# Kernel optimization log

Hardware: AMD Instinct MI355X
Metric: run time of the kernel (lower is better)

The kernel has to match this reference:

```python
import jax, jax.numpy as jnp
import numpy as np

B, N, C, H = 4, 128, 512, 8
D = C // H
SCALE = D ** (-0.5) * 50.0


def setup_inputs() -> dict:
    key = jax.random.key(0)
    kx, kw = jax.random.split(key)
    x = jax.random.normal(kx, (B, N, N, C), dtype=jnp.float32)
    # torch Linear(n_embd, 5*n_embd, bias=False); stored here as [in, out] for x @ w
    w_qkv = jax.random.normal(kw, (C, 5 * C), dtype=jnp.float32) * (C ** -0.5)
    return {"x": x, "w_qkv": w_qkv}


def _heads(t):
    # [b, i, j, h*d] -> [b, h, i, j, d]
    b, i, j, _ = t.shape
    return t.reshape(b, i, j, H, D).transpose(0, 3, 1, 2, 4)


def reference(x, w_qkv):
    # global norm over the entire tensor (torch .std() is unbiased, ddof=1)
    x = (x - x.mean()) / x.std(ddof=1)
    qkv = x @ w_qkv                                   # [b, i, j, 5c]
    q, k1, k2, v1, v2 = map(_heads, jnp.split(qkv, 5, axis=-1))
    # pivotal attention: for query (i,j), pivot over k with row stream k1[i,k]
    # and column stream k2[k,j]
    scores = SCALE * (jnp.einsum('bhijd,bhikd->bhijk', q, k1)
                      + jnp.einsum('bhijd,bhkjd->bhijk', q, k2))
    attn = jax.nn.softmax(scores, axis=-1)            # [b, h, i, j, k]
    out = (jnp.einsum('bhijk,bhikd->bhijd', attn, v1)
           + jnp.einsum('bhijk,bhkjd->bhijd', attn, v2))
    # [b, h, i, j, d] -> [b, i, j, h*d]
    return out.transpose(0, 2, 3, 1, 4).reshape(B, N, N, C)
```

## Files before the change

### kernel.cpp

```cpp
#include <hip/hip_runtime.h>
#include <stdint.h>


typedef __attribute__((ext_vector_type(8))) short s8v;
typedef __attribute__((ext_vector_type(4))) float f4v;

#define MFMA(a, b, c) __builtin_amdgcn_mfma_f32_16x16x32_bf16((a), (b), (c), 0, 0, 0)

__device__ __forceinline__ float bf2f(unsigned short u) {
  union { unsigned int i; float f; } v; v.i = ((unsigned int)u) << 16; return v.f;
}
__device__ __forceinline__ unsigned short f2bf(float f) {
  union { float f; unsigned int i; } v; v.f = f;
  unsigned int i = v.i;
  return (unsigned short)((i + 0x7fffu + ((i >> 16) & 1u)) >> 16);
}

__device__ __forceinline__ void async_copy16(const void* g, void* l) {
  __builtin_amdgcn_global_load_lds(
      (const __attribute__((address_space(1))) unsigned int*)(uintptr_t)g,
      (__attribute__((address_space(3))) unsigned int*)(uintptr_t)l,
      16, 0, 0);
}

__global__ __launch_bounds__(256) void k_probe(const unsigned short* __restrict__ x,
                                               int* __restrict__ flag) {
  uint4 v = ((const uint4*)x)[threadIdx.x];
  unsigned int uu[4] = {v.x, v.y, v.z, v.w};
  int bad = 0;
#pragma unroll
  for (int u = 0; u < 4; ++u) {
    float a = bf2f((unsigned short)(uu[u] & 0xffffu));
    float b = bf2f((unsigned short)(uu[u] >> 16));
    if (!(fabsf(a) <= 1e4f)) bad = 1;
    if (!(fabsf(b) <= 1e4f)) bad = 1;
  }
  if (bad) atomicOr(flag, 1);
}

__global__ __launch_bounds__(256) void k_red(const void* __restrict__ xraw,
                                             const int* __restrict__ flag,
                                             double* __restrict__ dstats) {
  __shared__ float red[8];
  const int fm = flag[0];
  int t = threadIdx.x;
  size_t gid = (size_t)blockIdx.x * 256 + t;
  float s = 0.f, ss = 0.f;
  if (fm) {
    const float4* pf = (const float4*)xraw;
#pragma unroll 4
    for (int it = 0; it < 32; ++it) {
      size_t idx = gid + (size_t)it * 131072;
      float4 u1 = pf[2 * idx], u2 = pf[2 * idx + 1];
      float vals[8] = {u1.x, u1.y, u1.z, u1.w, u2.x, u2.y, u2.z, u2.w};
#pragma unroll
      for (int u = 0; u < 8; ++u) { s += vals[u]; ss += vals[u] * vals[u]; }
    }
  } else {
    const uint4* p = (const uint4*)xraw;
#pragma unroll 4
    for (int it = 0; it < 32; ++it) {
      uint4 v = p[gid + (size_t)it * 131072];
      unsigned int uu[4] = {v.x, v.y, v.z, v.w};
#pragma unroll
      for (int u = 0; u < 4; ++u) {
        float a = bf2f((unsigned short)(uu[u] & 0xffffu));
        float b = bf2f((unsigned short)(uu[u] >> 16));
        s += a + b;
        ss += a * a + b * b;
      }
    }
  }
#pragma unroll
  for (int d = 32; d >= 1; d >>= 1) {
    s += __shfl_down(s, d);
    ss += __shfl_down(ss, d);
  }
  int lane = t & 63, wave = t >> 6;
  if (lane == 0) { red[wave] = s; red[4 + wave] = ss; }
  __syncthreads();
  if (t == 0) {
    atomicAdd(&dstats[0], (double)(red[0] + red[1] + red[2] + red[3]));
    atomicAdd(&dstats[1], (double)(red[4] + red[5] + red[6] + red[7]));
  }
}

__global__ void k_stats(const double* __restrict__ dstats, float* __restrict__ fstats) {
  double M = 33554432.0;
  double mean = dstats[0] / M;
  double var = (dstats[1] - dstats[0] * dstats[0] / M) / (M - 1.0);
  double istd = 1.0 / sqrt(var);
  fstats[0] = (float)istd;
  fstats[1] = (float)(-mean * istd);
}

__global__ __launch_bounds__(256) void k_colsum(const void* __restrict__ wraw,
                                                const int* __restrict__ flag,
                                                float* __restrict__ colsum) {
  const int fm = flag[0];
  int c = blockIdx.x * 256 + threadIdx.x;
  if (c >= 2560) return;
  float s = 0.f;
  if (fm) {
    const float* w = (const float*)wraw;
    for (int r = 0; r < 512; ++r) s += w[(size_t)r * 2560 + c];
  } else {
    const unsigned short* w = (const unsigned short*)wraw;
    for (int r = 0; r < 512; ++r) s += bf2f(w[(size_t)r * 2560 + c]);
  }
  colsum[c] = s;
}

__global__ __launch_bounds__(256) void k_wt(const void* __restrict__ wraw,
                                            const int* __restrict__ flag,
                                            unsigned short* __restrict__ wThi,
                                            unsigned short* __restrict__ wTlo) {
  __shared__ float tile[64][65];
  const int fm = flag[0];
  int n0 = blockIdx.x * 64, r0 = blockIdx.y * 64;
#pragma unroll
  for (int rep = 0; rep < 16; ++rep) {
    int idx = rep * 256 + threadIdx.x;
    int r = idx >> 6, n = idx & 63;
    float v;
    if (fm) v = ((const float*)wraw)[(size_t)(r0 + r) * 2560 + n0 + n];
    else    v = bf2f(((const unsigned short*)wraw)[(size_t)(r0 + r) * 2560 + n0 + n]);
    tile[r][n] = v;
  }
  __syncthreads();
#pragma unroll
  for (int rep = 0; rep < 16; ++rep) {
    int idx = rep * 256 + threadIdx.x;
    int n = idx >> 6, r = idx & 63;
    float v = tile[r][n];
    unsigned short hi = f2bf(v);
    size_t o = (size_t)(n0 + n) * 512 + r0 + r;
    wThi[o] = hi;
    wTlo[o] = f2bf(v - bf2f(hi));
  }
}

__global__ __launch_bounds__(256) void k_convx(const void* __restrict__ xraw,
                                               const int* __restrict__ flag,
                                               unsigned short* __restrict__ xhi,
                                               unsigned short* __restrict__ xlo,
                                               int b) {
  const int fm = flag[0];
  size_t e0 = ((size_t)blockIdx.x * 256 + threadIdx.x) * 8;
  size_t g0 = (size_t)b * 8388608 + e0;
  float vals[8];
  if (fm) {
    const float4* pf = (const float4*)xraw;
    float4 u1 = pf[g0 / 4], u2 = pf[g0 / 4 + 1];
    vals[0] = u1.x; vals[1] = u1.y; vals[2] = u1.z; vals[3] = u1.w;
    vals[4] = u2.x; vals[5] = u2.y; vals[6] = u2.z; vals[7] = u2.w;
  } else {
    uint4 v = ((const uint4*)xraw)[g0 / 8];
    unsigned int uu[4] = {v.x, v.y, v.z, v.w};
#pragma unroll
    for (int u = 0; u < 4; ++u) {
      vals[2 * u] = bf2f((unsigned short)(uu[u] & 0xffffu));
      vals[2 * u + 1] = bf2f((unsigned short)(uu[u] >> 16));
    }
  }
  unsigned short h[8], l[8];
#pragma unroll
  for (int u = 0; u < 8; ++u) {
    h[u] = f2bf(vals[u]);
    l[u] = f2bf(vals[u] - bf2f(h[u]));
  }
  *(uint4*)(xhi + e0) = *(const uint4*)h;
  *(uint4*)(xlo + e0) = *(const uint4*)l;
}

__global__ __launch_bounds__(256) void k_gemm(
    const unsigned short* __restrict__ xhi, const unsigned short* __restrict__ xlo,
    const unsigned short* __restrict__ wThi, const unsigned short* __restrict__ wTlo,
    const float* __restrict__ colsum, const float* __restrict__ fstats,
    const int* __restrict__ flag,
    unsigned short* __restrict__ qhi, unsigned short* __restrict__ qlo,
    unsigned short* __restrict__ k1hi, unsigned short* __restrict__ k1lo,
    unsigned short* __restrict__ k2hi, unsigned short* __restrict__ k2lo,
    unsigned short* __restrict__ v1T, unsigned short* __restrict__ v2T,
    int h0, int hcShift) {
  __shared__ __align__(16) unsigned short Ash[128 * 64];
  __shared__ __align__(16) unsigned short Asl[128 * 64];
  __shared__ __align__(16) unsigned short Bsh[128 * 64];
  __shared__ __align__(16) unsigned short Bsl[128 * 64];
  const int fm = flag[0];
  const int t = threadIdx.x;
  const int m0 = blockIdx.x * 128;
  const int n0 = blockIdx.y * 128;
  const int hcMask = (1 << hcShift) - 1;

  const int lane = t & 63, wave = t >> 6;
  const int wm = (wave & 1) * 64, wn = (wave >> 1) * 64;
  const int l16 = lane & 15, q4 = lane >> 4;
  const int srow = t >> 3;
  const int scol = (((t & 7) ^ ((t >> 3) & 7)) * 8);
  const int rsw = l16 & 7;

  const float af = fstats[0], bfc = fstats[1];
  const unsigned short* xh = xhi + (size_t)m0 * 512;
  const unsigned short* xl = xlo + (size_t)m0 * 512;

  int wcolr[4];
#pragma unroll
  for (int r = 0; r < 4; ++r) {
    int ncol = n0 + r * 32 + srow;
    int g = ncol >> hcShift, rem = ncol & hcMask;
    wcolr[r] = (g << 9) + ((h0 + (rem >> 6)) << 6) + (rem & 63);
  }

  f4v acc[4][4];
#pragma unroll
  for (int a = 0; a < 4; ++a)
#pragma unroll
    for (int c = 0; c < 4; ++c) acc[a][c] = (f4v)0.f;

  for (int k0 = 0; k0 < 512; k0 += 64) {
#pragma unroll
    for (int r = 0; r < 4; ++r) {
      int row = r * 32 + srow;
      async_copy16(xh + (size_t)row * 512 + k0 + scol, (char*)Ash + (r * 256 + t) * 16);
    }
#pragma unroll
    for (int r = 0; r < 4; ++r)
      async_copy16(wThi + (size_t)wcolr[r] * 512 + k0 + scol, (char*)Bsh + (r * 256 + t) * 16);
    if (fm) {
#pragma unroll
      for (int r = 0; r < 4; ++r) {
        int row = r * 32 + srow;
        async_copy16(xl + (size_t)row * 512 + k0 + scol, (char*)Asl + (r * 256 + t) * 16);
      }
#pragma unroll
      for (int r = 0; r < 4; ++r)
        async_copy16(wTlo + (size_t)wcolr[r] * 512 + k0 + scol, (char*)Bsl + (r * 256 + t) * 16);
    }
    __syncthreads();
#pragma unroll
    for (int kc = 0; kc < 2; ++kc) {
      const int swoff = ((kc * 4 + q4) ^ rsw) * 8;
      s8v ah[4], bh[4];
#pragma unroll
      for (int jt = 0; jt < 4; ++jt)
        ah[jt] = *(const s8v*)&Ash[(wm + jt * 16 + l16) * 64 + swoff];
#pragma unroll
      for (int nt = 0; nt < 4; ++nt)
        bh[nt] = *(const s8v*)&Bsh[(wn + nt * 16 + l16) * 64 + swoff];
      if (fm) {
        s8v al[4], bl[4];
#pragma unroll
        for (int jt = 0; jt < 4; ++jt)
          al[jt] = *(const s8v*)&Asl[(wm + jt * 16 + l16) * 64 + swoff];
#pragma unroll
        for (int nt = 0; nt < 4; ++nt)
          bl[nt] = *(const s8v*)&Bsl[(wn + nt * 16 + l16) * 64 + swoff];
#pragma unroll
        for (int jt = 0; jt < 4; ++jt)
#pragma unroll
          for (int nt = 0; nt < 4; ++nt) {
            acc[jt][nt] = MFMA(ah[jt], bh[nt], acc[jt][nt]);
            acc[jt][nt] = MFMA(ah[jt], bl[nt], acc[jt][nt]);
            acc[jt][nt] = MFMA(al[jt], bh[nt], acc[jt][nt]);
          }
      } else {
#pragma unroll
        for (int jt = 0; jt < 4; ++jt)
#pragma unroll
          for (int nt = 0; nt < 4; ++nt) acc[jt][nt] = MFMA(ah[jt], bh[nt], acc[jt][nt]);
      }
    }
    __syncthreads();
  }

#pragma unroll
  for (int jt = 0; jt < 4; ++jt) {
#pragma unroll
    for (int nt = 0; nt < 4; ++nt) {
      int gcol = n0 + wn + nt * 16 + l16;
      int g = gcol >> hcShift, rem = gcol & hcMask;
      int hl = rem >> 6, d = rem & 63;
      int wcol = (g << 9) + ((h0 + hl) << 6) + d;
      float cs = colsum[wcol] * bfc;
#pragma unroll
      for (int r = 0; r < 4; ++r) {
        int grow = m0 + wm + jt * 16 + q4 * 4 + r;
        int i = grow >> 7, j = grow & 127;
        float val = acc[jt][nt][r] * af + cs;
        unsigned short hi = f2bf(val);
        if (g == 0) {
          size_t idx = (((size_t)hl * 128 + i) * 128 + j) * 64 + d;
          qhi[idx] = hi; qlo[idx] = f2bf(val - bf2f(hi));
        } else if (g == 1) {
          size_t idx = (((size_t)hl * 128 + i) * 128 + j) * 64 + d;
          k1hi[idx] = hi; k1lo[idx] = f2bf(val - bf2f(hi));
        } else if (g == 2) {
          size_t idx = (((size_t)hl * 128 + j) * 128 + i) * 64 + d;
          k2hi[idx] = hi; k2lo[idx] = f2bf(val - bf2f(hi));
        } else if (g == 3) {
          size_t idx = (((size_t)hl * 128 + i) * 64 + d) * 128 + j;
          v1T[idx] = hi;
        } else {
          size_t idx = (((size_t)hl * 128 + j) * 64 + d) * 128 + i;
          v2T[idx] = hi;
        }
      }
    }
  }
}

__global__ __launch_bounds__(256) void k_s1(
    const unsigned short* __restrict__ qhi, const unsigned short* __restrict__ qlo,
    const unsigned short* __restrict__ k1hi, const unsigned short* __restrict__ k1lo,
    float* __restrict__ S) {
  const int i = blockIdx.x, hl = blockIdx.y;
  const int t = threadIdx.x, lane = t & 63, wave = t >> 6;
  const int l16 = lane & 15, q4 = lane >> 4;
  const size_t base = ((size_t)hl * 128 + i) * 128 * 64;

  f4v acc[2][8];
#pragma unroll
  for (int a = 0; a < 2; ++a)
#pragma unroll
    for (int c = 0; c < 8; ++c) acc[a][c] = (f4v)0.f;

#pragma unroll
  for (int kc = 0; kc < 2; ++kc) {
    s8v ah[2], al[2];
#pragma unroll
    for (int jt = 0; jt < 2; ++jt) {
      size_t off = base + (size_t)(wave * 32 + jt * 16 + l16) * 64 + kc * 32 + q4 * 8;
      ah[jt] = *(const s8v*)(qhi + off);
      al[jt] = *(const s8v*)(qlo + off);
    }
#pragma unroll
    for (int kt = 0; kt < 8; ++kt) {
      size_t off = base + (size_t)(kt * 16 + l16) * 64 + kc * 32 + q4 * 8;
      s8v bh = *(const s8v*)(k1hi + off);
      s8v bl = *(const s8v*)(k1lo + off);
#pragma unroll
      for (int jt = 0; jt < 2; ++jt) {
        acc[jt][kt] = MFMA(ah[jt], bh, acc[jt][kt]);
        acc[jt][kt] = MFMA(ah[jt], bl, acc[jt][kt]);
        acc[jt][kt] = MFMA(al[jt], bh, acc[jt][kt]);
      }
    }
  }
  float* Sb = S + ((size_t)hl * 128 + i) * 128 * 128;
#pragma unroll
  for (int jt = 0; jt < 2; ++jt)
#pragma unroll
    for (int kt = 0; kt < 8; ++kt)
#pragma unroll
      for (int r = 0; r < 4; ++r) {
        int j = wave * 32 + jt * 16 + q4 * 4 + r;
        Sb[(size_t)j * 128 + kt * 16 + l16] = acc[jt][kt][r];
      }
}

__global__ __launch_bounds__(256) void k_s2(
    const unsigned short* __restrict__ qhi, const unsigned short* __restrict__ qlo,
    const unsigned short* __restrict__ k2hi, const unsigned short* __restrict__ k2lo,
    const float* __restrict__ S, unsigned short* __restrict__ attn) {
  const int j = blockIdx.x, hl = blockIdx.y;
  const int t = threadIdx.x, lane = t & 63, wave = t >> 6;
  const int l16 = lane & 15, q4 = lane >> 4;
  const size_t bbase = ((size_t)hl * 128 + j) * 128 * 64;

  f4v acc[2][8];
#pragma unroll
  for (int a = 0; a < 2; ++a)
#pragma unroll
    for (int c = 0; c < 8; ++c) acc[a][c] = (f4v)0.f;

#pragma unroll
  for (int kc = 0; kc < 2; ++kc) {
    s8v ah[2], al[2];
#pragma unroll
    for (int it = 0; it < 2; ++it) {
      size_t off = (((size_t)hl * 128 + (wave * 32 + it * 16 + l16)) * 128 + j) * 64 +
                   kc * 32 + q4 * 8;
      ah[it] = *(const s8v*)(qhi + off);
      al[it] = *(const s8v*)(qlo + off);
    }
#pragma unroll
    for (int kt = 0; kt < 8; ++kt) {
      size_t off = bbase + (size_t)(kt * 16 + l16) * 64 + kc * 32 + q4 * 8;
      s8v bh = *(const s8v*)(k2hi + off);
      s8v bl = *(const s8v*)(k2lo + off);
#pragma unroll
      for (int it = 0; it < 2; ++it) {
        acc[it][kt] = MFMA(ah[it], bh, acc[it][kt]);
        acc[it][kt] = MFMA(ah[it], bl, acc[it][kt]);
        acc[it][kt] = MFMA(al[it], bh, acc[it][kt]);
      }
    }
  }

#pragma unroll
  for (int it = 0; it < 2; ++it) {
#pragma unroll
    for (int r = 0; r < 4; ++r) {
      int i = wave * 32 + it * 16 + q4 * 4 + r;
      const float* Srow = S + (((size_t)hl * 128 + i) * 128 + j) * 128;
      float tv[8];
      float m = -3.4e38f;
#pragma unroll
      for (int kt = 0; kt < 8; ++kt) {
        tv[kt] = 6.25f * (Srow[kt * 16 + l16] + acc[it][kt][r]);
        m = fmaxf(m, tv[kt]);
      }
#pragma unroll
      for (int d = 1; d <= 8; d <<= 1) m = fmaxf(m, __shfl_xor(m, d));
      float sum = 0.f;
#pragma unroll
      for (int kt = 0; kt < 8; ++kt) {
        tv[kt] = __expf(tv[kt] - m);
        sum += tv[kt];
      }
#pragma unroll
      for (int d = 1; d <= 8; d <<= 1) sum += __shfl_xor(sum, d);
      float rs = 1.f / sum;
      unsigned short* arow = attn + (((size_t)hl * 128 + i) * 128 + j) * 128;
#pragma unroll
      for (int kt = 0; kt < 8; ++kt) arow[kt * 16 + l16] = f2bf(tv[kt] * rs);
    }
  }
}

__global__ __launch_bounds__(256) void k_av1(
    const unsigned short* __restrict__ attn, const unsigned short* __restrict__ v1T,
    unsigned short* __restrict__ out1) {
  const int i = blockIdx.x, hl = blockIdx.y;
  const int t = threadIdx.x, lane = t & 63, wave = t >> 6;
  const int l16 = lane & 15, q4 = lane >> 4;
  const size_t abase = ((size_t)hl * 128 + i) * 128 * 128;
  const size_t vbase = ((size_t)hl * 128 + i) * 64 * 128;

  f4v acc[2][4];
#pragma unroll
  for (int a = 0; a < 2; ++a)
#pragma unroll
    for (int c = 0; c < 4; ++c) acc[a][c] = (f4v)0.f;

#pragma unroll
  for (int kc = 0; kc < 4; ++kc) {
    s8v a[2], bfr[4];
#pragma unroll
    for (int jt = 0; jt < 2; ++jt)
      a[jt] = *(const s8v*)(attn + abase + (size_t)(wave * 32 + jt * 16 + l16) * 128 +
                            kc * 32 + q4 * 8);
#pragma unroll
    for (int dt = 0; dt < 4; ++dt)
      bfr[dt] = *(const s8v*)(v1T + vbase + (size_t)(dt * 16 + l16) * 128 + kc * 32 + q4 * 8);
#pragma unroll
    for (int jt = 0; jt < 2; ++jt)
#pragma unroll
      for (int dt = 0; dt < 4; ++dt) acc[jt][dt] = MFMA(a[jt], bfr[dt], acc[jt][dt]);
  }
  unsigned short* ob = out1 + ((size_t)hl * 128 + i) * 128 * 64;
#pragma unroll
  for (int jt = 0; jt < 2; ++jt)
#pragma unroll
    for (int dt = 0; dt < 4; ++dt)
#pragma unroll
      for (int r = 0; r < 4; ++r) {
        int j = wave * 32 + jt * 16 + q4 * 4 + r;
        ob[(size_t)j * 64 + dt * 16 + l16] = f2bf(acc[jt][dt][r]);
      }
}

__global__ __launch_bounds__(256) void k_av2(
    const unsigned short* __restrict__ attn, const unsigned short* __restrict__ v2T,
    const unsigned short* __restrict__ out1, const int* __restrict__ flag,
    void* __restrict__ out, int b, int h0) {
  const int j = blockIdx.x, hl = blockIdx.y;
  const int t = threadIdx.x, lane = t & 63, wave = t >> 6;
  const int l16 = lane & 15, q4 = lane >> 4;
  const int fm = flag[0];
  const size_t vbase = ((size_t)hl * 128 + j) * 64 * 128;

  f4v acc[2][4];
#pragma unroll
  for (int a = 0; a < 2; ++a)
#pragma unroll
    for (int c = 0; c < 4; ++c) acc[a][c] = (f4v)0.f;

#pragma unroll
  for (int kc = 0; kc < 4; ++kc) {
    s8v a[2], bfr[4];
#pragma unroll
    for (int it = 0; it < 2; ++it)
      a[it] = *(const s8v*)(attn +
                            (((size_t)hl * 128 + (wave * 32 + it * 16 + l16)) * 128 + j) * 128 +
                            kc * 32 + q4 * 8);
#pragma unroll
    for (int dt = 0; dt < 4; ++dt)
      bfr[dt] = *(const s8v*)(v2T + vbase + (size_t)(dt * 16 + l16) * 128 + kc * 32 + q4 * 8);
#pragma unroll
    for (int it = 0; it < 2; ++it)
#pragma unroll
      for (int dt = 0; dt < 4; ++dt) acc[it][dt] = MFMA(a[it], bfr[dt], acc[it][dt]);
  }
#pragma unroll
  for (int it = 0; it < 2; ++it)
#pragma unroll
    for (int dt = 0; dt < 4; ++dt)
#pragma unroll
      for (int r = 0; r < 4; ++r) {
        int i = wave * 32 + it * 16 + q4 * 4 + r;
        int d = dt * 16 + l16;
        float o = acc[it][dt][r] + bf2f(out1[(((size_t)hl * 128 + i) * 128 + j) * 64 + d]);
        size_t oi = ((size_t)b * 16384 + i * 128 + j) * 512 + (h0 + hl) * 64 + d;
        if (fm) ((float*)out)[oi] = o;
        else    ((unsigned short*)out)[oi] = f2bf(o);
      }
}

extern "C" void kernel_launch(void* const* d_in, const int* in_sizes, int n_in,
                              void* d_out, int out_size, void* d_ws, size_t ws_size,
                              hipStream_t stream) {
  (void)in_sizes; (void)n_in; (void)out_size;
  const void* x = d_in[0];
  const void* w = d_in[1];

  const size_t xslice = (size_t)16384 * 512;
  const size_t wTsz = (size_t)2560 * 512;
  const size_t fixed = xslice * 4 + wTsz * 4 + 2560 * 4 + 64;

  int Hc = 2;
  if (30 * ((size_t)8 * 1048576) + fixed <= ws_size) Hc = 8;
  else if (30 * ((size_t)4 * 1048576) + fixed <= ws_size) Hc = 4;
  const int hcShift = (Hc == 8) ? 9 : ((Hc == 4) ? 8 : 7);
  const size_t TE = (size_t)Hc * 1048576;

  char* p = (char*)d_ws;
  unsigned short* qhi = (unsigned short*)p;  p += TE * 2;
  unsigned short* qlo = (unsigned short*)p;  p += TE * 2;
  unsigned short* k1hi = (unsigned short*)p; p += TE * 2;
  unsigned short* k1lo = (unsigned short*)p; p += TE * 2;
  unsigned short* k2hi = (unsigned short*)p; p += TE * 2;
  unsigned short* k2lo = (unsigned short*)p; p += TE * 2;
  unsigned short* v1T = (unsigned short*)p;  p += TE * 2;
  unsigned short* v2T = (unsigned short*)p;  p += TE * 2;
  float* S = (float*)p;                      p += TE * 8;
  unsigned short* attn = (unsigned short*)p; p += TE * 4;
  unsigned short* out1 = (unsigned short*)p; p += TE * 2;
  unsigned short* xhi = (unsigned short*)p;  p += xslice * 2;
  unsigned short* xlo = (unsigned short*)p;  p += xslice * 2;
  unsigned short* wThi = (unsigned short*)p; p += wTsz * 2;
  unsigned short* wTlo = (unsigned short*)p; p += wTsz * 2;
  float* colsum = (float*)p;                 p += 2560 * 4;
  double* dstats = (double*)p;               p += 16;
  int* flag = (int*)p;                       p += 8;
  float* fstats = (float*)p;                 p += 8;

  hipMemsetAsync(dstats, 0, 24, stream);
  k_probe<<<1, 256, 0, stream>>>((const unsigned short*)x, flag);
  k_red<<<512, 256, 0, stream>>>(x, flag, dstats);
  k_stats<<<1, 1, 0, stream>>>(dstats, fstats);
  k_colsum<<<10, 256, 0, stream>>>(w, flag, colsum);
  k_wt<<<dim3(40, 8), 256, 0, stream>>>(w, flag, wThi, wTlo);

  for (int b = 0; b < 4; ++b) {
    k_convx<<<4096, 256, 0, stream>>>(x, flag, xhi, xlo, b);
    for (int h0 = 0; h0 < 8; h0 += Hc) {
      k_gemm<<<dim3(128, (5 * Hc * 64) / 128), 256, 0, stream>>>(
          xhi, xlo, wThi, wTlo, colsum, fstats, flag,
          qhi, qlo, k1hi, k1lo, k2hi, k2lo, v1T, v2T, h0, hcShift);
      k_s1<<<dim3(128, Hc), 256, 0, stream>>>(qhi, qlo, k1hi, k1lo, S);
      k_s2<<<dim3(128, Hc), 256, 0, stream>>>(qhi, qlo, k2hi, k2lo, S, attn);
      k_av1<<<dim3(128, Hc), 256, 0, stream>>>(attn, v1T, out1);
      k_av2<<<dim3(128, Hc), 256, 0, stream>>>(attn, v2T, out1, flag, d_out, b, h0);
    }
  }
}
```

Measured before the change: 1.636 ms.

## Double-buffer QKV GEMM LDS tiles with 32-wide K steps

Restructures the projection GEMM main loop to use two LDS buffers with a K step of 32 instead of 64. The next tile's async global-to-LDS copies are issued before the MFMA work on the current buffer, removing one barrier per iteration and overlapping loads with compute. LDS footprint stays the same, but there are twice as many iterations and the swizzle pattern changes to a 4-chunk XOR scheme.

New measurement: 1.672 ms. 1.02x slower.

```diff
diff --git a/kernel.cpp b/kernel.cpp
--- a/kernel.cpp
+++ b/kernel.cpp
@@ -183,10 +183,10 @@
     unsigned short* __restrict__ k2hi, unsigned short* __restrict__ k2lo,
     unsigned short* __restrict__ v1T, unsigned short* __restrict__ v2T,
     int h0, int hcShift) {
-  __shared__ __align__(16) unsigned short Ash[128 * 64];
-  __shared__ __align__(16) unsigned short Asl[128 * 64];
-  __shared__ __align__(16) unsigned short Bsh[128 * 64];
-  __shared__ __align__(16) unsigned short Bsl[128 * 64];
+  __shared__ __align__(16) unsigned short Ash[2][4096];
+  __shared__ __align__(16) unsigned short Asl[2][4096];
+  __shared__ __align__(16) unsigned short Bsh[2][4096];
+  __shared__ __align__(16) unsigned short Bsl[2][4096];
   const int fm = flag[0];
   const int t = threadIdx.x;
   const int m0 = blockIdx.x * 128;
@@ -196,20 +196,22 @@
   const int lane = t & 63, wave = t >> 6;
   const int wm = (wave & 1) * 64, wn = (wave >> 1) * 64;
   const int l16 = lane & 15, q4 = lane >> 4;
-  const int srow = t >> 3;
-  const int scol = (((t & 7) ^ ((t >> 3) & 7)) * 8);
-  const int rsw = l16 & 7;
+
+  const int srow0 = t >> 2;
+  const int srow1 = 64 + srow0;
+  const int sch = (((t & 3) ^ ((t >> 3) & 3)) << 3);
+  const int swoff = ((q4 ^ ((l16 >> 1) & 3)) << 3);
 
   const float af = fstats[0], bfc = fstats[1];
   const unsigned short* xh = xhi + (size_t)m0 * 512;
   const unsigned short* xl = xlo + (size_t)m0 * 512;
 
-  int wcolr[4];
-#pragma unroll
-  for (int r = 0; r < 4; ++r) {
-    int ncol = n0 + r * 32 + srow;
-    int g = ncol >> hcShift, rem = ncol & hcMask;
-    wcolr[r] = (g << 9) + ((h0 + (rem >> 6)) << 6) + (rem & 63);
+  int wcol0, wcol1;
+  {
+    int n = n0 + srow0, g = n >> hcShift, rem = n & hcMask;
+    wcol0 = (g << 9) + ((h0 + (rem >> 6)) << 6) + (rem & 63);
+    n = n0 + srow1; g = n >> hcShift; rem = n & hcMask;
+    wcol1 = (g << 9) + ((h0 + (rem >> 6)) << 6) + (rem & 63);
   }
 
   f4v acc[4][4];
@@ -218,58 +220,55 @@
 #pragma unroll
     for (int c = 0; c < 4; ++c) acc[a][c] = (f4v)0.f;
 
-  for (int k0 = 0; k0 < 512; k0 += 64) {
-#pragma unroll
-    for (int r = 0; r < 4; ++r) {
-      int row = r * 32 + srow;
-      async_copy16(xh + (size_t)row * 512 + k0 + scol, (char*)Ash + (r * 256 + t) * 16);
-    }
-#pragma unroll
-    for (int r = 0; r < 4; ++r)
-      async_copy16(wThi + (size_t)wcolr[r] * 512 + k0 + scol, (char*)Bsh + (r * 256 + t) * 16);
+  auto STAGE = [&](int bsel, int k0) {
+    async_copy16(xh + (size_t)srow0 * 512 + k0 + sch, (char*)&Ash[bsel][0] + t * 16);
+    async_copy16(xh + (size_t)srow1 * 512 + k0 + sch, (char*)&Ash[bsel][0] + (256 + t) * 16);
+    async_copy16(wThi + (size_t)wcol0 * 512 + k0 + sch, (char*)&Bsh[bsel][0] + t * 16);
+    async_copy16(wThi + (size_t)wcol1 * 512 + k0 + sch, (char*)&Bsh[bsel][0] + (256 + t) * 16);
     if (fm) {
-#pragma unroll
-      for (int r = 0; r < 4; ++r) {
-        int row = r * 32 + srow;
-        async_copy16(xl + (size_t)row * 512 + k0 + scol, (char*)Asl + (r * 256 + t) * 16);
-      }
-#pragma unroll
-      for (int r = 0; r < 4; ++r)
-        async_copy16(wTlo + (size_t)wcolr[r] * 512 + k0 + scol, (char*)Bsl + (r * 256 + t) * 16);
-    }
-    __syncthreads();
-#pragma unroll
-    for (int kc = 0; kc < 2; ++kc) {
-      const int swoff = ((kc * 4 + q4) ^ rsw) * 8;
-      s8v ah[4], bh[4];
+      async_copy16(xl + (size_t)srow0 * 512 + k0 + sch, (char*)&Asl[bsel][0] + t * 16);
+      async_copy16(xl + (size_t)srow1 * 512 + k0 + sch, (char*)&Asl[bsel][0] + (256 + t) * 16);
+      async_copy16(wTlo + (size_t)wcol0 * 512 + k0 + sch, (char*)&Bsl[bsel][0] + t * 16);
+      async_copy16(wTlo + (size_t)wcol1 * 512 + k0 + sch, (char*)&Bsl[bsel][0] + (256 + t) * 16);
+    }
+  };
+
+  STAGE(0, 0);
+  __syncthreads();
+
+#pragma unroll 2
+  for (int ks = 0; ks < 16; ++ks) {
+    const int kb = ks & 1;
+    if (ks < 15) STAGE(kb ^ 1, (ks + 1) << 5);
+
+    s8v ah[4], bh[4];
+#pragma unroll
+    for (int jt = 0; jt < 4; ++jt)
+      ah[jt] = *(const s8v*)&Ash[kb][(wm + jt * 16 + l16) * 32 + swoff];
+#pragma unroll
+    for (int nt = 0; nt < 4; ++nt)
+      bh[nt] = *(const s8v*)&Bsh[kb][(wn + nt * 16 + l16) * 32 + swoff];
+    if (fm) {
+      s8v al[4], bl[4];
 #pragma unroll
       for (int jt = 0; jt < 4; ++jt)
-        ah[jt] = *(const s8v*)&Ash[(wm + jt * 16 + l16) * 64 + swoff];
+        al[jt] = *(const s8v*)&Asl[kb][(wm + jt * 16 + l16) * 32 + swoff];
 #pragma unroll
       for (int nt = 0; nt < 4; ++nt)
-        bh[nt] = *(const s8v*)&Bsh[(wn + nt * 16 + l16) * 64 + swoff];
-      if (fm) {
-        s8v al[4], bl[4];
-#pragma unroll
-        for (int jt = 0; jt < 4; ++jt)
-          al[jt] = *(const s8v*)&Asl[(wm + jt * 16 + l16) * 64 + swoff];
-#pragma unroll
-        for (int nt = 0; nt < 4; ++nt)
-          bl[nt] = *(const s8v*)&Bsl[(wn + nt * 16 + l16) * 64 + swoff];
-#pragma unroll
-        for (int jt = 0; jt < 4; ++jt)
-#pragma unroll
-          for (int nt = 0; nt < 4; ++nt) {
-            acc[jt][nt] = MFMA(ah[jt], bh[nt], acc[jt][nt]);
-            acc[jt][nt] = MFMA(ah[jt], bl[nt], acc[jt][nt]);
-            acc[jt][nt] = MFMA(al[jt], bh[nt], acc[jt][nt]);
-          }
-      } else {
-#pragma unroll
-        for (int jt = 0; jt < 4; ++jt)
-#pragma unroll
-          for (int nt = 0; nt < 4; ++nt) acc[jt][nt] = MFMA(ah[jt], bh[nt], acc[jt][nt]);
-      }
+        bl[nt] = *(const s8v*)&Bsl[kb][(wn + nt * 16 + l16) * 32 + swoff];
+#pragma unroll
+      for (int jt = 0; jt < 4; ++jt)
+#pragma unroll
+        for (int nt = 0; nt < 4; ++nt) {
+          acc[jt][nt] = MFMA(ah[jt], bh[nt], acc[jt][nt]);
+          acc[jt][nt] = MFMA(ah[jt], bl[nt], acc[jt][nt]);
+          acc[jt][nt] = MFMA(al[jt], bh[nt], acc[jt][nt]);
+        }
+    } else {
+#pragma unroll
+      for (int jt = 0; jt < 4; ++jt)
+#pragma unroll
+        for (int nt = 0; nt < 4; ++nt) acc[jt][nt] = MFMA(ah[jt], bh[nt], acc[jt][nt]);
     }
     __syncthreads();
   }
```
